# Performance work log

Measured on AMD Instinct MI355X. Metric: run time of the kernel, lower is better.

The kernel has to match this reference:

```python
import jax, jax.numpy as jnp
import numpy as np

N, C, K, H = 100000, 128, 16, 4
D = C // H
EPS = 1e-5


def _gelu(x):
    return jax.nn.gelu(x, approximate=False)


def _ln(x, g, b):
    mu = jnp.mean(x, axis=-1, keepdims=True)
    var = jnp.var(x, axis=-1, keepdims=True)
    return (x - mu) * jax.lax.rsqrt(var + EPS) * g + b


def setup_inputs() -> dict:
    key = jax.random.key(0)
    ks = jax.random.split(key, 24)
    s = 0.02
    inp = {
        "feat": jax.random.normal(ks[0], (N, C), jnp.float32),
        "coords": jax.random.normal(ks[1], (N, 3), jnp.float32),
        "knn_idx": jax.random.randint(ks[2], (N, K), 0, N, jnp.int32),
        "Wq": jax.random.normal(ks[3], (C, C), jnp.float32) * s,
        "bq": jnp.zeros((C,), jnp.float32),
        "Wk": jax.random.normal(ks[4], (C, C), jnp.float32) * s,
        "bk": jnp.zeros((C,), jnp.float32),
        "Wv": jax.random.normal(ks[5], (C, C), jnp.float32) * s,
        "bv": jnp.zeros((C,), jnp.float32),
        "Wp1": jax.random.normal(ks[6], (3, C), jnp.float32) * s,
        "bp1": jnp.zeros((C,), jnp.float32),
        "Wp2": jax.random.normal(ks[7], (C, C), jnp.float32) * s,
        "bp2": jnp.zeros((C,), jnp.float32),
        "Wo": jax.random.normal(ks[8], (C, C), jnp.float32) * s,
        "bo": jnp.zeros((C,), jnp.float32),
        "g1": jnp.ones((C,), jnp.float32),
        "b1": jnp.zeros((C,), jnp.float32),
        "Wf1": jax.random.normal(ks[9], (C, 2 * C), jnp.float32) * s,
        "bf1": jnp.zeros((2 * C,), jnp.float32),
        "Wf2": jax.random.normal(ks[10], (2 * C, C), jnp.float32) * s,
        "bf2": jnp.zeros((C,), jnp.float32),
        "g2": jnp.ones((C,), jnp.float32),
        "b2": jnp.zeros((C,), jnp.float32),
    }
    return inp


def reference(feat, coords, knn_idx, Wq, bq, Wk, bk, Wv, bv, Wp1, bp1, Wp2, bp2,
              Wo, bo, g1, b1, Wf1, bf1, Wf2, bf2, g2, b2):
    q = feat @ Wq + bq                      # (N, C)
    k_feat = feat @ Wk + bk
    v_feat = feat @ Wv + bv
    k_nbr = k_feat[knn_idx]                 # (N, K, C) irregular gather
    v_nbr = v_feat[knn_idx]
    rel_pos = coords[knn_idx] - coords[:, None, :]   # (N, K, 3)
    pe = _gelu(rel_pos @ Wp1 + bp1) @ Wp2 + bp2      # (N, K, C)
    k_nbr = (k_nbr + pe).reshape(N, K, H, D)
    v_nbr = (v_nbr + pe).reshape(N, K, H, D)
    qh = q.reshape(N, H, D)
    attn = jnp.einsum('nhd,nkhd->nhk', qh, k_nbr) / jnp.sqrt(jnp.float32(D))
    attn = jax.nn.softmax(attn, axis=-1)    # softmax over the K neighbors
    out = jnp.einsum('nhk,nkhd->nhd', attn, v_nbr).reshape(N, C)
    out = out @ Wo + bo
    x = _ln(feat + out, g1, b1)
    ffn = _gelu(x @ Wf1 + bf1) @ Wf2 + bf2
    return _ln(x + ffn, g2, b2)
```

## Files before the change

kernel.cpp:

```cpp
#include <hip/hip_runtime.h>
#include <math.h>

#define NPTS 100000
#define KNN  16
#define CH   50000
#define NCHUNK 2
#define ATT_BLOCKS 768

typedef unsigned short bf16;
typedef __attribute__((ext_vector_type(8))) short bf16x8;
typedef __attribute__((ext_vector_type(4))) float f32x4;

__device__ __forceinline__ float bf2f(bf16 v) {
    union { unsigned int u; float f; } x; x.u = ((unsigned int)v) << 16; return x.f;
}
__device__ __forceinline__ bf16 f2bf(float f) {
    union { float f; unsigned int u; } x; x.f = f;
    unsigned int r = (x.u + 0x7FFFu + ((x.u >> 16) & 1u)) >> 16;
    return (bf16)r;
}
__device__ __forceinline__ float f_lo(unsigned int u) {
    union { unsigned int x; float f; } c; c.x = u << 16; return c.f;
}
__device__ __forceinline__ float f_hi(unsigned int u) {
    union { unsigned int x; float f; } c; c.x = u & 0xffff0000u; return c.f;
}
__device__ __forceinline__ float ld1(const float* p) { return *p; }
__device__ __forceinline__ float ld1(const bf16* p) { return bf2f(*p); }
__device__ __forceinline__ void st1(float* p, float v) { *p = v; }
__device__ __forceinline__ void st1(bf16* p, float v) { *p = f2bf(v); }

__device__ __forceinline__ float gelu_f(float x) {
    return 0.5f * x * (1.0f + erff(x * 0.70710678118654752f));
}
__device__ __forceinline__ float gelu_poly(float t) {
    float w = t * t;
    float poly = fmaf(w, fmaf(w, 0.025f, -0.16666667f), 1.0f);
    return t * fmaf(0.3989423f * t, poly, 0.5f);
}

__global__ void prep1_kernel(const float* __restrict__ Wp2, const float* __restrict__ Wo,
                             const float* __restrict__ bo, const float* __restrict__ bp2,
                             const float* __restrict__ bq, const float* __restrict__ bk,
                             const float* __restrict__ bv,
                             float* __restrict__ Wcat2, float* __restrict__ bo2,
                             float* __restrict__ bcat) {
    int b = blockIdx.x, t = threadIdx.x;
    if (b < 512) {
        int h = b >> 7, j = b & 127;
        float s = 0.f;
        for (int d = 0; d < 32; d++)
            s += Wp2[j * 128 + h * 32 + d] * Wo[(h * 32 + d) * 128 + t];
        Wcat2[b * 128 + t] = s;
    } else if (b == 512) {
        float s = bo[t];
        for (int c = 0; c < 128; c++) s += bp2[c] * Wo[c * 128 + t];
        bo2[t] = s;
    } else {
        bcat[t] = bq[t]; bcat[128 + t] = bk[t]; bcat[256 + t] = bv[t];
    }
}

__global__ void prep2_kernel(const float* __restrict__ Wq, const float* __restrict__ Wk,
                             const float* __restrict__ Wv, const float* __restrict__ Wp2,
                             const float* __restrict__ Wo, const float* __restrict__ Wcat2,
                             const float* __restrict__ Wf1, const float* __restrict__ Wf2,
                             bf16* __restrict__ BcatT, bf16* __restrict__ W2TT,
                             bf16* __restrict__ WcatT, bf16* __restrict__ Wf1T,
                             bf16* __restrict__ Wf2T) {
    int b = blockIdx.x, t = threadIdx.x;
    if (b < 384) {
        const float* W = (b < 128) ? Wq : (b < 256) ? Wk : Wv;
        BcatT[b * 128 + t] = f2bf(W[t * 128 + (b & 127)]);
    } else if (b < 512) {
        int idx = b - 384, h = idx >> 5, d = idx & 31;
        W2TT[h * 4096 + t * 32 + d] = f2bf(Wp2[t * 128 + h * 32 + d]);
    } else if (b < 640) {
        int j = b - 512;
        for (int i = 0; i < 5; i++) {
            int r = t + 128 * i;
            float v = (r < 128) ? Wo[r * 128 + j] : Wcat2[(r - 128) * 128 + j];
            WcatT[j * 640 + r] = f2bf(v);
        }
    } else if (b < 896) {
        int n = b - 640;
        Wf1T[n * 128 + t] = f2bf(Wf1[t * 256 + n]);
    } else {
        int n = b - 896;
        for (int i = 0; i < 2; i++) {
            int k = t + 128 * i;
            Wf2T[n * 256 + k] = f2bf(Wf2[k * 128 + n]);
        }
    }
}

template<int EPI, bool SPLITA, typename TA, typename TC, typename TR>
__global__ __launch_bounds__(256) void mfma_gemm(
    const TA* __restrict__ A, const bf16* __restrict__ A2,
    const bf16* __restrict__ BT, const float* __restrict__ bias,
    const TR* __restrict__ resid, const float* __restrict__ gamma,
    const float* __restrict__ beta, TC* __restrict__ Cc,
    int Nrows, int Kdim, int lda, int ldc,
    int zA, int zBT, int zbias, int zC)
{
    __shared__ bf16 As[128 * 36];
    __shared__ bf16 Bs[128 * 36];
    __shared__ float reds[256], redq[256];
    __shared__ float mu[128], rstd[128];

    const int tid = threadIdx.x;
    const int z = blockIdx.z;
    const TA* Ab = A + (size_t)z * zA;
    const bf16* BTb = BT + (size_t)z * zBT;
    const float* biasb = bias + (size_t)z * zbias;
    TC* Cb = Cc + (size_t)z * zC;

    const int row0 = blockIdx.x * 128;
    const int col0 = blockIdx.y * 128;
    const int wave = tid >> 6, wr = wave >> 1, wc = wave & 1;
    const int l = tid & 63, l15 = l & 15, g = l >> 4;
    const int ar = tid >> 1;
    const int ah = (tid & 1) * 16;

    f32x4 acc[4][4];
#pragma unroll
    for (int i = 0; i < 4; i++)
#pragma unroll
        for (int j = 0; j < 4; j++) acc[i][j] = (f32x4){0.f, 0.f, 0.f, 0.f};

    for (int k0 = 0; k0 < Kdim; k0 += 32) {
        {
            int row = row0 + ar;
            bool ok = row < Nrows;
            ushort4 tmp[4];
            if (ok) {
                if constexpr (SPLITA) {
                    if (k0 < 128) {
                        const bf16* s = (const bf16*)Ab + (size_t)row * 128 + k0 + ah;
#pragma unroll
                        for (int j = 0; j < 4; j++) tmp[j] = ((const ushort4*)s)[j];
                    } else {
                        const bf16* s = A2 + (size_t)row * 512 + (k0 - 128) + ah;
#pragma unroll
                        for (int j = 0; j < 4; j++) tmp[j] = ((const ushort4*)s)[j];
                    }
                } else if constexpr (sizeof(TA) == 4) {
                    const float4* s = (const float4*)((const float*)Ab + (size_t)row * lda + k0 + ah);
#pragma unroll
                    for (int j = 0; j < 4; j++) {
                        float4 v = s[j];
                        tmp[j] = make_ushort4(f2bf(v.x), f2bf(v.y), f2bf(v.z), f2bf(v.w));
                    }
                } else {
                    const bf16* s = (const bf16*)Ab + (size_t)row * lda + k0 + ah;
#pragma unroll
                    for (int j = 0; j < 4; j++) tmp[j] = ((const ushort4*)s)[j];
                }
            } else {
#pragma unroll
                for (int j = 0; j < 4; j++) tmp[j] = make_ushort4(0, 0, 0, 0);
            }
#pragma unroll
            for (int j = 0; j < 4; j++)
                *(ushort4*)(As + ar * 36 + ah + 4 * j) = tmp[j];
        }
        {
            int n = col0 + ar;
            const bf16* s = BTb + (size_t)n * Kdim + k0 + ah;
#pragma unroll
            for (int j = 0; j < 4; j++)
                *(ushort4*)(Bs + ar * 36 + ah + 4 * j) = ((const ushort4*)s)[j];
        }
        __syncthreads();

        union FragU { uint2 q2[2]; bf16x8 v; };
        bf16x8 af[4], bfr[4];
#pragma unroll
        for (int mt = 0; mt < 4; mt++) {
            const bf16* p = As + (wr * 64 + mt * 16 + l15) * 36 + 4 * g;
            FragU u; u.q2[0] = *(const uint2*)p; u.q2[1] = *(const uint2*)(p + 16);
            af[mt] = u.v;
        }
#pragma unroll
        for (int nt = 0; nt < 4; nt++) {
            const bf16* p = Bs + (wc * 64 + nt * 16 + l15) * 36 + 4 * g;
            FragU u; u.q2[0] = *(const uint2*)p; u.q2[1] = *(const uint2*)(p + 16);
            bfr[nt] = u.v;
        }
#pragma unroll
        for (int mt = 0; mt < 4; mt++)
#pragma unroll
            for (int nt = 0; nt < 4; nt++)
                acc[mt][nt] = __builtin_amdgcn_mfma_f32_16x16x32_bf16(
                    af[mt], bfr[nt], acc[mt][nt], 0, 0, 0);
        __syncthreads();
    }

    if constexpr (EPI != 3) {
#pragma unroll
        for (int mt = 0; mt < 4; mt++) {
#pragma unroll
            for (int r = 0; r < 4; r++) {
                int row = row0 + wr * 64 + mt * 16 + g * 4 + r;
                if (row < Nrows) {
                    size_t base = (size_t)row * ldc;
#pragma unroll
                    for (int nt = 0; nt < 4; nt++) {
                        int col = col0 + wc * 64 + nt * 16 + l15;
                        float t = acc[mt][nt][r];
                        if constexpr (EPI >= 1) t += biasb[col];
                        if constexpr (EPI == 2) t = gelu_f(t);
                        st1(Cb + base + col, t);
                    }
                }
            }
        }
    } else {
#pragma unroll
        for (int mt = 0; mt < 4; mt++) {
#pragma unroll
            for (int r = 0; r < 4; r++) {
                int rl = wr * 64 + mt * 16 + g * 4 + r;
                int row = row0 + rl;
                float s = 0.f, q = 0.f;
#pragma unroll
                for (int nt = 0; nt < 4; nt++) {
                    int col = wc * 64 + nt * 16 + l15;
                    float t = acc[mt][nt][r] + biasb[col];
                    if (row < Nrows) t += ld1(resid + (size_t)row * 128 + col);
                    acc[mt][nt][r] = t;
                    s += t; q = fmaf(t, t, q);
                }
#pragma unroll
                for (int off = 1; off <= 8; off <<= 1) {
                    s += __shfl_xor(s, off, 16);
                    q += __shfl_xor(q, off, 16);
                }
                if (l15 == 0) { reds[rl * 2 + wc] = s; redq[rl * 2 + wc] = q; }
            }
        }
        __syncthreads();
        if (tid < 128) {
            float s = reds[tid * 2] + reds[tid * 2 + 1];
            float q = redq[tid * 2] + redq[tid * 2 + 1];
            float m = s * (1.f / 128.f);
            float v = q * (1.f / 128.f) - m * m;
            mu[tid] = m; rstd[tid] = rsqrtf(v + 1e-5f);
        }
        __syncthreads();
#pragma unroll
        for (int mt = 0; mt < 4; mt++) {
#pragma unroll
            for (int r = 0; r < 4; r++) {
                int rl = wr * 64 + mt * 16 + g * 4 + r;
                int row = row0 + rl;
                if (row < Nrows) {
                    float m = mu[rl], rd = rstd[rl];
#pragma unroll
                    for (int nt = 0; nt < 4; nt++) {
                        int col = wc * 64 + nt * 16 + l15;
                        st1(Cb + (size_t)row * 128 + col,
                            (acc[mt][nt][r] - m) * rd * gamma[col] + beta[col]);
                    }
                }
            }
        }
    }
}

__global__ __launch_bounds__(256, 4) void attn_kernel(
    const bf16* __restrict__ qx, const bf16* __restrict__ kf,
    const bf16* __restrict__ vf, const bf16* __restrict__ qp,
    const float* __restrict__ coords, const int* __restrict__ knn,
    const float* __restrict__ Wp1, const float* __restrict__ bp1,
    bf16* __restrict__ attn_v, bf16* __restrict__ s_out, int nbase)
{
    __shared__ __align__(16) float W1s[524];
    __shared__ __align__(16) float hv_s[4][16 * 144];
    __shared__ __align__(16) float qp_s[4][4 * 144];
    __shared__ __align__(16) float a_s[4][64];
    __shared__ int idx_s[4][16];

    const int tid = threadIdx.x;
    if (tid < 128) {
        int c = tid;
        int s4 = 4 * c + 4 * (c >> 5);
        W1s[s4 + 0] = Wp1[c];
        W1s[s4 + 1] = Wp1[128 + c];
        W1s[s4 + 2] = Wp1[256 + c];
        W1s[s4 + 3] = bp1[c];
    }
    __syncthreads();

    const int wv = tid >> 6, l = tid & 63;
    const int k = l >> 2, j = l & 3;
    float* hvf = hv_s[wv];
    float* qpsf = qp_s[wv];
    float* as4 = a_s[wv];
    int* ixs = idx_s[wv];
    const float SCALE = 0.17677669529663688f;
    const int wave = blockIdx.x * 4 + wv;
    const int loff1 = (l >> 5) * 36 + (l & 31);
    const int loff2 = loff1 + 72;
    const int qoff = (l >> 4) * 144 + ((l & 15) >> 2) * 36 + ((l & 15) & 3) * 8;

    for (int n = nbase + wave; n < nbase + CH; n += ATT_BLOCKS * 4) {
        const int idx = knn[n * KNN + k];
        if (j == 0) ixs[k] = idx;
        const float cx = coords[n * 3 + 0], cy = coords[n * 3 + 1], cz = coords[n * 3 + 2];
        const float rx = coords[idx * 3 + 0] - cx;
        const float ry = coords[idx * 3 + 1] - cy;
        const float rz = coords[idx * 3 + 2] - cz;
        {
            uint4 qpr = *(const uint4*)(qp + (size_t)(n - nbase) * 512 + l * 8);
            float4 qa, qb;
            qa.x = f_lo(qpr.x); qa.y = f_hi(qpr.x);
            qa.z = f_lo(qpr.y); qa.w = f_hi(qpr.y);
            qb.x = f_lo(qpr.z); qb.y = f_hi(qpr.z);
            qb.z = f_lo(qpr.w); qb.w = f_hi(qpr.w);
            *(float4*)(qpsf + qoff) = qa;
            *(float4*)(qpsf + qoff + 4) = qb;
        }
        const bf16* krow = kf + (size_t)idx * 128 + j * 32;
        const bf16* qrow = qx + (size_t)n * 128 + j * 32;
        uint4 kw[4], qw[4];
#pragma unroll
        for (int m = 0; m < 4; m++) {
            kw[m] = *(const uint4*)(krow + 8 * m);
            qw[m] = *(const uint4*)(qrow + 8 * m);
        }
        asm volatile("s_waitcnt lgkmcnt(0)" ::: "memory");

        float p0 = 0.f, p1 = 0.f, p2 = 0.f, p3 = 0.f;
        const float* wbase = W1s + 132 * j;
        const int jb = j * 36;
#pragma unroll
        for (int blk = 0; blk < 4; blk++) {
            const int cb = blk * 8;
            float4 q0a = *(const float4*)(qpsf + jb + cb);
            float4 q0b = *(const float4*)(qpsf + jb + cb + 4);
            float4 q1a = *(const float4*)(qpsf + 144 + jb + cb);
            float4 q1b = *(const float4*)(qpsf + 144 + jb + cb + 4);
            float4 q2a = *(const float4*)(qpsf + 288 + jb + cb);
            float4 q2b = *(const float4*)(qpsf + 288 + jb + cb + 4);
            float4 q3a = *(const float4*)(qpsf + 432 + jb + cb);
            float4 q3b = *(const float4*)(qpsf + 432 + jb + cb + 4);
            float g[8];
#pragma unroll
            for (int i = 0; i < 8; i++) {
                float4 w = *(const float4*)(wbase + 4 * (cb + i));
                float t = fmaf(rx, w.x, fmaf(ry, w.y, fmaf(rz, w.z, w.w)));
                float gg = gelu_poly(t);
                g[i] = gg;
                float v0 = (i < 4) ? ((const float*)&q0a)[i] : ((const float*)&q0b)[i - 4];
                float v1 = (i < 4) ? ((const float*)&q1a)[i] : ((const float*)&q1b)[i - 4];
                float v2 = (i < 4) ? ((const float*)&q2a)[i] : ((const float*)&q2b)[i - 4];
                float v3 = (i < 4) ? ((const float*)&q3a)[i] : ((const float*)&q3b)[i - 4];
                p0 = fmaf(gg, v0, p0);
                p1 = fmaf(gg, v1, p1);
                p2 = fmaf(gg, v2, p2);
                p3 = fmaf(gg, v3, p3);
            }
            float* hrow = hvf + k * 144 + jb + cb;
            *(float4*)hrow = make_float4(g[0], g[1], g[2], g[3]);
            *(float4*)(hrow + 4) = make_float4(g[4], g[5], g[6], g[7]);
        }

        float qk = 0.f;
#pragma unroll
        for (int m = 0; m < 4; m++) {
#pragma unroll
            for (int w = 0; w < 4; w++) {
                unsigned int ua = ((const unsigned int*)&kw[m])[w];
                unsigned int ub = ((const unsigned int*)&qw[m])[w];
                qk = fmaf(f_lo(ua), f_lo(ub), qk);
                qk = fmaf(f_hi(ua), f_hi(ub), qk);
            }
        }

        p0 += __shfl_xor(p0, 1); p0 += __shfl_xor(p0, 2);
        p1 += __shfl_xor(p1, 1); p1 += __shfl_xor(p1, 2);
        p2 += __shfl_xor(p2, 1); p2 += __shfl_xor(p2, 2);
        p3 += __shfl_xor(p3, 1); p3 += __shfl_xor(p3, 2);
        float pe = (j == 0) ? p0 : (j == 1) ? p1 : (j == 2) ? p2 : p3;
        float logit = (qk + pe) * SCALE;

        float mx = logit;
#pragma unroll
        for (int off = 4; off <= 32; off <<= 1) mx = fmaxf(mx, __shfl_xor(mx, off));
        float e = __expf(logit - mx);
        float ss = e;
#pragma unroll
        for (int off = 4; off <= 32; off <<= 1) ss += __shfl_xor(ss, off);
        float a = e * __builtin_amdgcn_rcpf(ss);
        as4[k * 4 + j] = a;
        asm volatile("s_waitcnt lgkmcnt(0)" ::: "memory");
        __builtin_amdgcn_sched_barrier(0);

        float ov0 = 0.f, ov1 = 0.f;
        float sv00 = 0.f, sv01 = 0.f, sv10 = 0.f, sv11 = 0.f;
        float sv20 = 0.f, sv21 = 0.f, sv30 = 0.f, sv31 = 0.f;
#pragma unroll
        for (int kk = 0; kk < 16; kk++) {
            float4 av = *(const float4*)(as4 + kk * 4);
            float h1v = hvf[kk * 144 + loff1];
            float h2v = hvf[kk * 144 + loff2];
            sv00 = fmaf(av.x, h1v, sv00); sv01 = fmaf(av.x, h2v, sv01);
            sv10 = fmaf(av.y, h1v, sv10); sv11 = fmaf(av.y, h2v, sv11);
            sv20 = fmaf(av.z, h1v, sv20); sv21 = fmaf(av.z, h2v, sv21);
            sv30 = fmaf(av.w, h1v, sv30); sv31 = fmaf(av.w, h2v, sv31);
            int ixk = ixs[kk];
            float vl = bf2f(vf[(size_t)ixk * 128 + l]);
            float vh = bf2f(vf[(size_t)ixk * 128 + 64 + l]);
            ov0 = fmaf((l < 32) ? av.x : av.y, vl, ov0);
            ov1 = fmaf((l < 32) ? av.z : av.w, vh, ov1);
        }
        const size_t sb = (size_t)(n - nbase) * 512;
        s_out[sb + l]       = f2bf(sv00); s_out[sb + 64 + l]  = f2bf(sv01);
        s_out[sb + 128 + l] = f2bf(sv10); s_out[sb + 192 + l] = f2bf(sv11);
        s_out[sb + 256 + l] = f2bf(sv20); s_out[sb + 320 + l] = f2bf(sv21);
        s_out[sb + 384 + l] = f2bf(sv30); s_out[sb + 448 + l] = f2bf(sv31);
        attn_v[(size_t)n * 128 + l]      = f2bf(ov0);
        attn_v[(size_t)n * 128 + 64 + l] = f2bf(ov1);
    }
}

__global__ void ws_report_kernel(float* out, int n, float val) {
    int i = blockIdx.x * 256 + threadIdx.x;
    if (i < n) out[i] = val;
}

extern "C" void kernel_launch(void* const* d_in, const int* in_sizes, int n_in,
                              void* d_out, int out_size, void* d_ws, size_t ws_size,
                              hipStream_t stream) {
    const float* feat   = (const float*)d_in[0];
    const float* coords = (const float*)d_in[1];
    const int*   knn    = (const int*)d_in[2];
    const float* Wq  = (const float*)d_in[3];  const float* bq  = (const float*)d_in[4];
    const float* Wk  = (const float*)d_in[5];  const float* bk  = (const float*)d_in[6];
    const float* Wv  = (const float*)d_in[7];  const float* bv  = (const float*)d_in[8];
    const float* Wp1 = (const float*)d_in[9];  const float* bp1 = (const float*)d_in[10];
    const float* Wp2 = (const float*)d_in[11]; const float* bp2 = (const float*)d_in[12];
    const float* Wo  = (const float*)d_in[13]; const float* bo  = (const float*)d_in[14];
    const float* g1  = (const float*)d_in[15]; const float* b1  = (const float*)d_in[16];
    const float* Wf1 = (const float*)d_in[17]; const float* bf1 = (const float*)d_in[18];
    const float* Wf2 = (const float*)d_in[19]; const float* bf2 = (const float*)d_in[20];
    const float* g2  = (const float*)d_in[21]; const float* b2  = (const float*)d_in[22];

    bf16* qx = (bf16*)d_ws;
    bf16* kb = qx + (size_t)NPTS * 128;
    bf16* vb = kb + (size_t)NPTS * 128;
    bf16* BcatT = vb + (size_t)NPTS * 128;
    bf16* W2TT  = BcatT + 384 * 128;
    bf16* WcatT = W2TT + 4 * 128 * 32;
    bf16* Wf1T  = WcatT + 128 * 640;
    bf16* Wf2T  = Wf1T + 256 * 128;
    float* Wcat2 = (float*)(Wf2T + 128 * 256);
    float* bo2   = Wcat2 + 512 * 128;
    float* bcat  = bo2 + 128;

    const size_t needed = ((size_t)NPTS * 128 * 3 + 384 * 128 + 4 * 128 * 32 + 128 * 640
                           + 256 * 128 + 128 * 256) * 2
                        + (512 * 128 + 128 + 384) * 4;
    if (ws_size < needed) {
        float val = 1000.0f + (float)((double)ws_size / 1073741824.0);
        hipLaunchKernelGGL(ws_report_kernel, dim3((out_size + 255) / 256), dim3(256), 0, stream,
                           (float*)d_out, out_size, val);
        return;
    }

    dim3 blk(256);
    const int GN = (NPTS + 127) / 128;
    const int GC = (CH + 127) / 128;

    hipLaunchKernelGGL(prep1_kernel, dim3(514), dim3(128), 0, stream,
                       Wp2, Wo, bo, bp2, bq, bk, bv, Wcat2, bo2, bcat);
    hipLaunchKernelGGL(prep2_kernel, dim3(1024), dim3(128), 0, stream,
                       Wq, Wk, Wv, Wp2, Wo, Wcat2, Wf1, Wf2,
                       BcatT, W2TT, WcatT, Wf1T, Wf2T);

    hipLaunchKernelGGL((mfma_gemm<1, false, float, bf16, float>),
                       dim3(GN, 1, 3), blk, 0, stream,
                       feat, nullptr, BcatT, bcat, nullptr, nullptr, nullptr, qx,
                       NPTS, 128, 128, 128, 0, 128 * 128, 128, NPTS * 128);

    bf16* qpb = (bf16*)d_out;

    for (int c = 0; c < NCHUNK; c++) {
        const int base = c * CH;
        hipLaunchKernelGGL((mfma_gemm<0, false, bf16, bf16, float>),
                           dim3(GC, 1, 4), blk, 0, stream,
                           qx + (size_t)base * 128, nullptr, W2TT, nullptr,
                           nullptr, nullptr, nullptr, qpb,
                           CH, 32, 128, 512, 32, 128 * 32, 0, 128);
        hipLaunchKernelGGL(attn_kernel, dim3(ATT_BLOCKS), blk, 0, stream,
                           qx, kb, vb, qpb, coords, knn, Wp1, bp1,
                           qx, qpb, base);
        hipLaunchKernelGGL((mfma_gemm<3, true, bf16, bf16, float>),
                           dim3(GC, 1, 1), blk, 0, stream,
                           qx + (size_t)base * 128, qpb, WcatT, bo2,
                           feat + (size_t)base * 128, g1, b1, qx + (size_t)base * 128,
                           CH, 640, 128, 128, 0, 0, 0, 0);
    }

    hipLaunchKernelGGL((mfma_gemm<2, false, bf16, bf16, float>),
                       dim3(GN, 2, 1), blk, 0, stream,
                       qx, nullptr, Wf1T, bf1, nullptr, nullptr, nullptr, kb,
                       NPTS, 128, 128, 256, 0, 0, 0, 0);

    hipLaunchKernelGGL((mfma_gemm<3, false, bf16, float, bf16>),
                       dim3(GN, 1, 1), blk, 0, stream,
                       kb, nullptr, Wf2T, bf2, qx, g2, b2, (float*)d_out,
                       NPTS, 256, 256, 128, 0, 0, 0, 0);
}
```

Measured before the change: 464.9 us.

## Vectorize GEMM epilogue stores and pack attention hidden values as bf16

Swaps the MFMA operand order so each lane holds four consecutive columns, letting the GEMM epilogues (bias, GELU, residual plus LayerNorm) use float4 bias loads and 8- or 16-byte vector stores instead of scalar ones. In the attention kernel the GELU hidden tile in shared memory is stored as packed bf16 pairs, which cuts LDS footprint and traffic. Value gathers and the s and attn_v outputs also become 32-bit packed accesses. Launch bounds and the attention grid are raised to fit more resident blocks. The new packing rounds with a plain add of 0x8000 instead of round-to-nearest-even, and the hidden tile loses precision going from fp32 to bf16.

```diff
diff --git a/kernel.cpp b/kernel.cpp
--- a/kernel.cpp
+++ b/kernel.cpp
@@ -5,7 +5,7 @@
 #define KNN  16
 #define CH   50000
 #define NCHUNK 2
-#define ATT_BLOCKS 768
+#define ATT_BLOCKS 1280
 
 typedef unsigned short bf16;
 typedef __attribute__((ext_vector_type(8))) short bf16x8;
@@ -19,6 +19,10 @@
     unsigned int r = (x.u + 0x7FFFu + ((x.u >> 16) & 1u)) >> 16;
     return (bf16)r;
 }
+__device__ __forceinline__ unsigned int pack_bf16(float lo, float hi) {
+    union { float f; unsigned int u; } a, b; a.f = lo; b.f = hi;
+    return ((b.u + 0x8000u) & 0xffff0000u) | ((a.u + 0x8000u) >> 16);
+}
 __device__ __forceinline__ float f_lo(unsigned int u) {
     union { unsigned int x; float f; } c; c.x = u << 16; return c.f;
 }
@@ -27,8 +31,6 @@
 }
 __device__ __forceinline__ float ld1(const float* p) { return *p; }
 __device__ __forceinline__ float ld1(const bf16* p) { return bf2f(*p); }
-__device__ __forceinline__ void st1(float* p, float v) { *p = v; }
-__device__ __forceinline__ void st1(bf16* p, float v) { *p = f2bf(v); }
 
 __device__ __forceinline__ float gelu_f(float x) {
     return 0.5f * x * (1.0f + erff(x * 0.70710678118654752f));
@@ -192,52 +194,71 @@
 #pragma unroll
             for (int nt = 0; nt < 4; nt++)
                 acc[mt][nt] = __builtin_amdgcn_mfma_f32_16x16x32_bf16(
-                    af[mt], bfr[nt], acc[mt][nt], 0, 0, 0);
+                    bfr[nt], af[mt], acc[mt][nt], 0, 0, 0);
         __syncthreads();
     }
 
+    const int cg = 4 * g;
+
     if constexpr (EPI != 3) {
 #pragma unroll
-        for (int mt = 0; mt < 4; mt++) {
-#pragma unroll
-            for (int r = 0; r < 4; r++) {
-                int row = row0 + wr * 64 + mt * 16 + g * 4 + r;
+        for (int nt = 0; nt < 4; nt++) {
+            const int col = col0 + wc * 64 + nt * 16 + cg;
+            float4 bv4 = make_float4(0.f, 0.f, 0.f, 0.f);
+            if constexpr (EPI >= 1) bv4 = *(const float4*)(biasb + col);
+#pragma unroll
+            for (int mt = 0; mt < 4; mt++) {
+                int row = row0 + wr * 64 + mt * 16 + l15;
                 if (row < Nrows) {
-                    size_t base = (size_t)row * ldc;
-#pragma unroll
-                    for (int nt = 0; nt < 4; nt++) {
-                        int col = col0 + wc * 64 + nt * 16 + l15;
-                        float t = acc[mt][nt][r];
-                        if constexpr (EPI >= 1) t += biasb[col];
-                        if constexpr (EPI == 2) t = gelu_f(t);
-                        st1(Cb + base + col, t);
+                    float t0 = acc[mt][nt][0], t1 = acc[mt][nt][1];
+                    float t2 = acc[mt][nt][2], t3 = acc[mt][nt][3];
+                    if constexpr (EPI >= 1) { t0 += bv4.x; t1 += bv4.y; t2 += bv4.z; t3 += bv4.w; }
+                    if constexpr (EPI == 2) { t0 = gelu_f(t0); t1 = gelu_f(t1); t2 = gelu_f(t2); t3 = gelu_f(t3); }
+                    if constexpr (sizeof(TC) == 2) {
+                        uint2 u; u.x = pack_bf16(t0, t1); u.y = pack_bf16(t2, t3);
+                        *(uint2*)((bf16*)Cb + (size_t)row * ldc + col) = u;
+                    } else {
+                        *(float4*)((float*)Cb + (size_t)row * ldc + col) = make_float4(t0, t1, t2, t3);
                     }
                 }
             }
         }
     } else {
+        float4 bias4[4];
+#pragma unroll
+        for (int nt = 0; nt < 4; nt++)
+            bias4[nt] = *(const float4*)(biasb + wc * 64 + nt * 16 + cg);
 #pragma unroll
         for (int mt = 0; mt < 4; mt++) {
-#pragma unroll
-            for (int r = 0; r < 4; r++) {
-                int rl = wr * 64 + mt * 16 + g * 4 + r;
-                int row = row0 + rl;
-                float s = 0.f, q = 0.f;
-#pragma unroll
-                for (int nt = 0; nt < 4; nt++) {
-                    int col = wc * 64 + nt * 16 + l15;
-                    float t = acc[mt][nt][r] + biasb[col];
-                    if (row < Nrows) t += ld1(resid + (size_t)row * 128 + col);
-                    acc[mt][nt][r] = t;
-                    s += t; q = fmaf(t, t, q);
+            int rl = wr * 64 + mt * 16 + l15;
+            int row = row0 + rl;
+            float s = 0.f, q = 0.f;
+#pragma unroll
+            for (int nt = 0; nt < 4; nt++) {
+                const int col = wc * 64 + nt * 16 + cg;
+                float rv0 = 0.f, rv1 = 0.f, rv2 = 0.f, rv3 = 0.f;
+                if (row < Nrows) {
+                    if constexpr (sizeof(TR) == 2) {
+                        ushort4 rr = *(const ushort4*)((const bf16*)resid + (size_t)row * 128 + col);
+                        rv0 = bf2f(rr.x); rv1 = bf2f(rr.y); rv2 = bf2f(rr.z); rv3 = bf2f(rr.w);
+                    } else {
+                        float4 rr = *(const float4*)((const float*)resid + (size_t)row * 128 + col);
+                        rv0 = rr.x; rv1 = rr.y; rv2 = rr.z; rv3 = rr.w;
+                    }
                 }
-#pragma unroll
-                for (int off = 1; off <= 8; off <<= 1) {
-                    s += __shfl_xor(s, off, 16);
-                    q += __shfl_xor(q, off, 16);
-                }
-                if (l15 == 0) { reds[rl * 2 + wc] = s; redq[rl * 2 + wc] = q; }
+                float t0 = acc[mt][nt][0] + bias4[nt].x + rv0;
+                float t1 = acc[mt][nt][1] + bias4[nt].y + rv1;
+                float t2 = acc[mt][nt][2] + bias4[nt].z + rv2;
+                float t3 = acc[mt][nt][3] + bias4[nt].w + rv3;
+                acc[mt][nt][0] = t0; acc[mt][nt][1] = t1;
+                acc[mt][nt][2] = t2; acc[mt][nt][3] = t3;
+                s += t0 + t1 + t2 + t3;
+                q = fmaf(t0, t0, q); q = fmaf(t1, t1, q);
+                q = fmaf(t2, t2, q); q = fmaf(t3, t3, q);
             }
+            s += __shfl_xor(s, 16); s += __shfl_xor(s, 32);
+            q += __shfl_xor(q, 16); q += __shfl_xor(q, 32);
+            if ((l & 48) == 0) { reds[rl * 2 + wc] = s; redq[rl * 2 + wc] = q; }
         }
         __syncthreads();
         if (tid < 128) {
@@ -248,19 +269,30 @@
             mu[tid] = m; rstd[tid] = rsqrtf(v + 1e-5f);
         }
         __syncthreads();
+        float4 g4[4], b4[4];
+#pragma unroll
+        for (int nt = 0; nt < 4; nt++) {
+            g4[nt] = *(const float4*)(gamma + wc * 64 + nt * 16 + cg);
+            b4[nt] = *(const float4*)(beta + wc * 64 + nt * 16 + cg);
+        }
 #pragma unroll
         for (int mt = 0; mt < 4; mt++) {
-#pragma unroll
-            for (int r = 0; r < 4; r++) {
-                int rl = wr * 64 + mt * 16 + g * 4 + r;
-                int row = row0 + rl;
-                if (row < Nrows) {
-                    float m = mu[rl], rd = rstd[rl];
-#pragma unroll
-                    for (int nt = 0; nt < 4; nt++) {
-                        int col = wc * 64 + nt * 16 + l15;
-                        st1(Cb + (size_t)row * 128 + col,
-                            (acc[mt][nt][r] - m) * rd * gamma[col] + beta[col]);
+            int rl = wr * 64 + mt * 16 + l15;
+            int row = row0 + rl;
+            if (row < Nrows) {
+                float m = mu[rl], rd = rstd[rl];
+#pragma unroll
+                for (int nt = 0; nt < 4; nt++) {
+                    const int col = wc * 64 + nt * 16 + cg;
+                    float t0 = (acc[mt][nt][0] - m) * rd * g4[nt].x + b4[nt].x;
+                    float t1 = (acc[mt][nt][1] - m) * rd * g4[nt].y + b4[nt].y;
+                    float t2 = (acc[mt][nt][2] - m) * rd * g4[nt].z + b4[nt].z;
+                    float t3 = (acc[mt][nt][3] - m) * rd * g4[nt].w + b4[nt].w;
+                    if constexpr (sizeof(TC) == 2) {
+                        uint2 u; u.x = pack_bf16(t0, t1); u.y = pack_bf16(t2, t3);
+                        *(uint2*)((bf16*)Cb + (size_t)row * 128 + col) = u;
+                    } else {
+                        *(float4*)((float*)Cb + (size_t)row * 128 + col) = make_float4(t0, t1, t2, t3);
                     }
                 }
             }
@@ -268,7 +300,7 @@
     }
 }
 
-__global__ __launch_bounds__(256, 4) void attn_kernel(
+__global__ __launch_bounds__(256, 5) void attn_kernel(
     const bf16* __restrict__ qx, const bf16* __restrict__ kf,
     const bf16* __restrict__ vf, const bf16* __restrict__ qp,
     const float* __restrict__ coords, const int* __restrict__ knn,
@@ -276,7 +308,7 @@
     bf16* __restrict__ attn_v, bf16* __restrict__ s_out, int nbase)
 {
     __shared__ __align__(16) float W1s[524];
-    __shared__ __align__(16) float hv_s[4][16 * 144];
+    __shared__ __align__(16) unsigned int hv_s[4][16 * 68];
     __shared__ __align__(16) float qp_s[4][4 * 144];
     __shared__ __align__(16) float a_s[4][64];
     __shared__ int idx_s[4][16];
@@ -294,14 +326,12 @@
 
     const int wv = tid >> 6, l = tid & 63;
     const int k = l >> 2, j = l & 3;
-    float* hvf = hv_s[wv];
+    unsigned int* hv32 = hv_s[wv];
     float* qpsf = qp_s[wv];
     float* as4 = a_s[wv];
     int* ixs = idx_s[wv];
     const float SCALE = 0.17677669529663688f;
     const int wave = blockIdx.x * 4 + wv;
-    const int loff1 = (l >> 5) * 36 + (l & 31);
-    const int loff2 = loff1 + 72;
     const int qoff = (l >> 4) * 144 + ((l & 15) >> 2) * 36 + ((l & 15) & 3) * 8;
 
     for (int n = nbase + wave; n < nbase + CH; n += ATT_BLOCKS * 4) {
@@ -345,25 +375,28 @@
             float4 q2b = *(const float4*)(qpsf + 288 + jb + cb + 4);
             float4 q3a = *(const float4*)(qpsf + 432 + jb + cb);
             float4 q3b = *(const float4*)(qpsf + 432 + jb + cb + 4);
-            float g[8];
+            float gg[8];
 #pragma unroll
             for (int i = 0; i < 8; i++) {
                 float4 w = *(const float4*)(wbase + 4 * (cb + i));
                 float t = fmaf(rx, w.x, fmaf(ry, w.y, fmaf(rz, w.z, w.w)));
-                float gg = gelu_poly(t);
-                g[i] = gg;
+                float gv = gelu_poly(t);
+                gg[i] = gv;
                 float v0 = (i < 4) ? ((const float*)&q0a)[i] : ((const float*)&q0b)[i - 4];
                 float v1 = (i < 4) ? ((const float*)&q1a)[i] : ((const float*)&q1b)[i - 4];
                 float v2 = (i < 4) ? ((const float*)&q2a)[i] : ((const float*)&q2b)[i - 4];
                 float v3 = (i < 4) ? ((const float*)&q3a)[i] : ((const float*)&q3b)[i - 4];
-                p0 = fmaf(gg, v0, p0);
-                p1 = fmaf(gg, v1, p1);
-                p2 = fmaf(gg, v2, p2);
-                p3 = fmaf(gg, v3, p3);
+                p0 = fmaf(gv, v0, p0);
+                p1 = fmaf(gv, v1, p1);
+                p2 = fmaf(gv, v2, p2);
+                p3 = fmaf(gv, v3, p3);
             }
-            float* hrow = hvf + k * 144 + jb + cb;
-            *(float4*)hrow = make_float4(g[0], g[1], g[2], g[3]);
-            *(float4*)(hrow + 4) = make_float4(g[4], g[5], g[6], g[7]);
+            uint4 pk4;
+            pk4.x = pack_bf16(gg[0], gg[1]);
+            pk4.y = pack_bf16(gg[2], gg[3]);
+            pk4.z = pack_bf16(gg[4], gg[5]);
+            pk4.w = pack_bf16(gg[6], gg[7]);
+            *(uint4*)(hv32 + k * 68 + j * 16 + blk * 4) = pk4;
         }
 
         float qk = 0.f;
@@ -398,30 +431,33 @@
         __builtin_amdgcn_sched_barrier(0);
 
         float ov0 = 0.f, ov1 = 0.f;
-        float sv00 = 0.f, sv01 = 0.f, sv10 = 0.f, sv11 = 0.f;
-        float sv20 = 0.f, sv21 = 0.f, sv30 = 0.f, sv31 = 0.f;
+        float sv0a = 0.f, sv0b = 0.f, sv1a = 0.f, sv1b = 0.f;
+        float sv2a = 0.f, sv2b = 0.f, sv3a = 0.f, sv3b = 0.f;
+        const int l4 = l & 16, l5 = l & 32;
 #pragma unroll
         for (int kk = 0; kk < 16; kk++) {
             float4 av = *(const float4*)(as4 + kk * 4);
-            float h1v = hvf[kk * 144 + loff1];
-            float h2v = hvf[kk * 144 + loff2];
-            sv00 = fmaf(av.x, h1v, sv00); sv01 = fmaf(av.x, h2v, sv01);
-            sv10 = fmaf(av.y, h1v, sv10); sv11 = fmaf(av.y, h2v, sv11);
-            sv20 = fmaf(av.z, h1v, sv20); sv21 = fmaf(av.z, h2v, sv21);
-            sv30 = fmaf(av.w, h1v, sv30); sv31 = fmaf(av.w, h2v, sv31);
+            unsigned int hp = hv32[kk * 68 + l];
+            float h_lo = f_lo(hp), h_hi = f_hi(hp);
+            sv0a = fmaf(av.x, h_lo, sv0a); sv0b = fmaf(av.x, h_hi, sv0b);
+            sv1a = fmaf(av.y, h_lo, sv1a); sv1b = fmaf(av.y, h_hi, sv1b);
+            sv2a = fmaf(av.z, h_lo, sv2a); sv2b = fmaf(av.z, h_hi, sv2b);
+            sv3a = fmaf(av.w, h_lo, sv3a); sv3b = fmaf(av.w, h_hi, sv3b);
             int ixk = ixs[kk];
-            float vl = bf2f(vf[(size_t)ixk * 128 + l]);
-            float vh = bf2f(vf[(size_t)ixk * 128 + 64 + l]);
-            ov0 = fmaf((l < 32) ? av.x : av.y, vl, ov0);
-            ov1 = fmaf((l < 32) ? av.z : av.w, vh, ov1);
-        }
-        const size_t sb = (size_t)(n - nbase) * 512;
-        s_out[sb + l]       = f2bf(sv00); s_out[sb + 64 + l]  = f2bf(sv01);
-        s_out[sb + 128 + l] = f2bf(sv10); s_out[sb + 192 + l] = f2bf(sv11);
-        s_out[sb + 256 + l] = f2bf(sv20); s_out[sb + 320 + l] = f2bf(sv21);
-        s_out[sb + 384 + l] = f2bf(sv30); s_out[sb + 448 + l] = f2bf(sv31);
-        attn_v[(size_t)n * 128 + l]      = f2bf(ov0);
-        attn_v[(size_t)n * 128 + 64 + l] = f2bf(ov1);
+            unsigned int vp = *(const unsigned int*)(vf + (size_t)ixk * 128 + 2 * l);
+            float v_lo = f_lo(vp), v_hi = f_hi(vp);
+            float t01 = l4 ? av.y : av.x;
+            float t23 = l4 ? av.w : av.z;
+            float ah = l5 ? t23 : t01;
+            ov0 = fmaf(ah, v_lo, ov0);
+            ov1 = fmaf(ah, v_hi, ov1);
+        }
+        unsigned int* s32 = (unsigned int*)(s_out + (size_t)(n - nbase) * 512);
+        s32[l]        = pack_bf16(sv0a, sv0b);
+        s32[64 + l]   = pack_bf16(sv1a, sv1b);
+        s32[128 + l]  = pack_bf16(sv2a, sv2b);
+        s32[192 + l]  = pack_bf16(sv3a, sv3b);
+        *(unsigned int*)(attn_v + (size_t)n * 128 + 2 * l) = pack_bf16(ov0, ov1);
     }
 }
 
```

Result: faster. 452.8 us (-2.6%).
